# Optimization experiments

Hardware: AMD Instinct MI355X
Metric: run time of the kernel (lower is better)

Reference implementation:

```python
import jax, jax.numpy as jnp
import numpy as np

NUM_PRODUCT = 100000
NUM_USERS = 10000
EMBED_DIM = 512
H = EMBED_DIM // 2          # gru_hidden_size = embedding_dim // 2
MBS = 20                    # max_basket_size
NB = 64                     # baskets per user
K = 256                     # batch of users
B = NB * MBS                # flattened item positions per user
L = 2                       # GRU layers


def setup_inputs() -> dict:
    key = jax.random.key(0)
    ks = jax.random.split(key, 8)
    filter_basket_prob = jax.random.uniform(ks[0], (K, B), dtype=jnp.float32)
    # item ids in [-1, NUM_PRODUCT-1]; -1 is padding (shifted to padding_idx 0)
    input_seq_tensor = jax.random.randint(ks[1], (K, B), 0, NUM_PRODUCT + 1) - 1
    uid = jax.random.randint(ks[2], (K,), 0, NUM_USERS)
    embed_table = 0.02 * jax.random.normal(ks[3], (NUM_PRODUCT + 1, H), dtype=jnp.float32)
    embed_table = embed_table.at[0].set(0.0)  # padding_idx=0
    s = 1.0 / np.sqrt(H)
    w_ih = jax.random.uniform(ks[4], (L, 3 * H, H), jnp.float32, -s, s)
    w_hh = jax.random.uniform(ks[5], (L, 3 * H, H), jnp.float32, -s, s)
    b_ih = jax.random.uniform(ks[6], (L, 3 * H), jnp.float32, -s, s)
    b_hh = jax.random.uniform(ks[7], (L, 3 * H), jnp.float32, -s, s)
    return {"filter_basket_prob": filter_basket_prob, "input_seq_tensor": input_seq_tensor,
            "uid": uid, "embed_table": embed_table,
            "w_ih": w_ih, "w_hh": w_hh, "b_ih": b_ih, "b_hh": b_hh}


def _gru_layer(x, wih, whh, bih, bhh):
    # x: [K, T, H]; torch GRU gate math (r, z, n gate order)
    gi = jnp.einsum('kth,gh->ktg', x, wih) + bih  # [K, T, 3H]

    def step(h, gi_t):
        gh = h @ whh.T + bhh
        ir, iz, inn = jnp.split(gi_t, 3, axis=-1)
        hr, hz, hn = jnp.split(gh, 3, axis=-1)
        r = jax.nn.sigmoid(ir + hr)
        z = jax.nn.sigmoid(iz + hz)
        n = jnp.tanh(inn + r * hn)
        h_new = (1.0 - z) * n + z * h
        return h_new, h_new

    h0 = jnp.zeros((x.shape[0], whh.shape[1]), x.dtype)
    _, hs = jax.lax.scan(step, h0, jnp.swapaxes(gi, 0, 1))  # [T, K, H]
    return jnp.swapaxes(hs, 0, 1)


def reference(filter_basket_prob, input_seq_tensor, uid, embed_table, w_ih, w_hh, b_ih, b_hh):
    Kb, Bb = filter_basket_prob.shape
    Hh = embed_table.shape[1]
    nb = Bb // MBS
    # mask out padding positions (constant w.r.t. grads, as in torch .detach())
    mask = (input_seq_tensor != -1).astype(jnp.float32)
    prob = filter_basket_prob * mask                      # [K, B]
    emb = embed_table[input_seq_tensor + 1]               # [K, B, H]
    emb_f = (emb * prob[..., None]).reshape(Kb, nb, MBS, Hh)
    prob_b = prob.reshape(Kb, nb, MBS)
    filter_b = prob_b.max(axis=-1)                        # [K, NB]
    # avg basket pooling: sum(prob*emb) / (sum(prob) + eps)
    basket_emb = emb_f.sum(axis=2) / (prob_b.sum(axis=-1, keepdims=True) + 1e-10)
    valid = (filter_b > 0).astype(jnp.int32)
    # stable descending sort moves valid baskets to the front, preserving order
    order = jnp.argsort(-valid, axis=-1)                  # [K, NB]
    lengths = valid.sum(axis=-1)
    lengths = lengths + (lengths == 0).astype(lengths.dtype)  # clamp to >= 1
    x = jnp.take_along_axis(basket_emb, order[:, :, None], axis=1)  # [K, NB, H]
    # pack/pad/unsort in the original cancel out: GRU output at t depends only
    # on inputs <= t, so run the full padded scan and read step lengths-1.
    for l in range(w_ih.shape[0]):
        x = _gru_layer(x, w_ih[l], w_hh[l], b_ih[l], b_hh[l])
    return x[jnp.arange(Kb), lengths - 1]                 # [K, H]
```

## Files before the change

### kernel.cpp

```cpp
#include <hip/hip_runtime.h>
#include <cstdint>

#define KU 256
#define NBASK 64
#define MBS 20
#define BITEMS 1280
#define HD 256
#define G3 768
#define TT 64

typedef short v8s __attribute__((ext_vector_type(8)));
typedef float v4f __attribute__((ext_vector_type(4)));
typedef unsigned short v4us __attribute__((ext_vector_type(4)));
typedef unsigned int v4u __attribute__((ext_vector_type(4)));

__device__ __forceinline__ unsigned short f2b(float f){
  uint32_t u = __float_as_uint(f);
  u += 0x7FFFu + ((u >> 16) & 1u);
  return (unsigned short)(u >> 16);
}
__device__ __forceinline__ float b2f(unsigned short s){
  return __uint_as_float(((uint32_t)s) << 16);
}
__device__ __forceinline__ unsigned int packf(float x){
  unsigned short hi = f2b(x);
  unsigned short lo = f2b(x - b2f(hi));
  return ((unsigned int)hi << 16) | lo;
}
__device__ __forceinline__ float unpackf(unsigned int v){
  return b2f((unsigned short)(v >> 16)) + b2f((unsigned short)(v & 0xffffu));
}

__global__ __launch_bounds__(1024) void k_convert(
    const float* __restrict__ wih, const float* __restrict__ whh,
    unsigned short* __restrict__ wih1hi, unsigned short* __restrict__ wih1lo,
    unsigned short* __restrict__ wih2hi, unsigned short* __restrict__ wih2lo,
    unsigned short* __restrict__ whh1hi, unsigned short* __restrict__ whh1lo,
    unsigned short* __restrict__ whh2hi, unsigned short* __restrict__ whh2lo)
{
  int idx = blockIdx.x * 1024 + threadIdx.x;
  int which = blockIdx.y;
  float v;
  if (which == 0)      v = wih[idx];
  else if (which == 1) v = wih[196608 + idx];
  else if (which == 2) v = whh[idx];
  else                 v = whh[196608 + idx];
  unsigned short hi = f2b(v);
  unsigned short lo = f2b(v - b2f(hi));
  if (which == 0)      { wih1hi[idx] = hi; wih1lo[idx] = lo; }
  else if (which == 1) { wih2hi[idx] = hi; wih2lo[idx] = lo; }
  else if (which == 2) { whh1hi[idx] = hi; whh1lo[idx] = lo; }
  else                 { whh2hi[idx] = hi; whh2lo[idx] = lo; }
}

__global__ void k_zero(int* flags){
  if (threadIdx.x < 32) flags[threadIdx.x] = 0;
}

__global__ __launch_bounds__(64) void k_order(
    const float* __restrict__ prob, const int* __restrict__ seq,
    int* __restrict__ order, int* __restrict__ lengths)
{
  int k = blockIdx.x, j = threadIdx.x;
  int base = k * BITEMS + j * MBS;
  float mx = 0.f;
  #pragma unroll
  for (int m = 0; m < MBS; m++) {
    int it = seq[base + m];
    float p = (it >= 0) ? prob[base + m] : 0.f;
    mx = fmaxf(mx, p);
  }
  bool valid = mx > 0.f;
  unsigned long long bal = __ballot(valid);
  int len = __popcll(bal);
  unsigned long long below = bal & ((1ull << j) - 1ull);
  int pos = valid ? __popcll(below) : (len + (j - __popcll(below)));
  order[k * NBASK + j] = pos;
  if (j == 0) lengths[k] = (len > 0) ? len : 1;
}

__global__ __launch_bounds__(256) void k_basket(
    const float* __restrict__ prob, const int* __restrict__ seq,
    const float* __restrict__ table, const int* __restrict__ order,
    unsigned short* __restrict__ xbhi, unsigned short* __restrict__ xblo)
{
  int j = blockIdx.x, k = blockIdx.y;
  int h = threadIdx.x;
  int base = k * BITEMS + j * MBS;
  float acc = 0.f, sp = 0.f;
  #pragma unroll
  for (int m = 0; m < MBS; m++) {
    int it = seq[base + m];
    if (it >= 0) {
      float p = prob[base + m];
      sp += p;
      acc += p * table[(size_t)(it + 1) * HD + h];
    }
  }
  float val = acc / (sp + 1e-10f);
  int dest = order[k * NBASK + j];
  unsigned short hi = f2b(val);
  size_t o = ((size_t)k * NBASK + dest) * HD + h;
  xbhi[o] = hi;
  xblo[o] = f2b(val - b2f(hi));
}

__global__ __launch_bounds__(256) void k_gemm3(
    const unsigned short* __restrict__ Xhi, const unsigned short* __restrict__ Xlo,
    const unsigned short* __restrict__ Whi, const unsigned short* __restrict__ Wlo,
    const float* __restrict__ bias, float* __restrict__ Y)
{
  int nblk = blockIdx.x;
  int mblk = blockIdx.y;
  int wv = threadIdx.x >> 6;
  int l = threadIdx.x & 63;
  int r = l & 15, g = l >> 4;
  int mbase = mblk * 64 + wv * 16;
  int nbase = nblk * 64;
  v4f acc[4];
  #pragma unroll
  for (int c = 0; c < 4; c++) {
    float bn = bias[nbase + c * 16 + r];
    acc[c] = (v4f){bn, bn, bn, bn};
  }
  const unsigned short* xh = Xhi + (size_t)(mbase + r) * HD;
  const unsigned short* xl = Xlo + (size_t)(mbase + r) * HD;
  #pragma unroll
  for (int k0 = 0; k0 < HD; k0 += 32) {
    v8s ahi = *(const v8s*)(xh + k0 + g * 8);
    v8s alo = *(const v8s*)(xl + k0 + g * 8);
    #pragma unroll
    for (int c = 0; c < 4; c++) {
      size_t wo = (size_t)(nbase + c * 16 + r) * HD + k0 + g * 8;
      v8s bhi = *(const v8s*)(Whi + wo);
      v8s blo = *(const v8s*)(Wlo + wo);
      acc[c] = __builtin_amdgcn_mfma_f32_16x16x32_bf16(ahi, bhi, acc[c], 0, 0, 0);
      acc[c] = __builtin_amdgcn_mfma_f32_16x16x32_bf16(alo, bhi, acc[c], 0, 0, 0);
      acc[c] = __builtin_amdgcn_mfma_f32_16x16x32_bf16(ahi, blo, acc[c], 0, 0, 0);
    }
  }
  #pragma unroll
  for (int c = 0; c < 4; c++) {
    int n = nbase + c * 16 + r;
    int mrow = mbase + g * 4;
    #pragma unroll
    for (int i = 0; i < 4; i++)
      Y[(size_t)(mrow + i) * G3 + n] = acc[c][i];
  }
}

__device__ __forceinline__ void mfma_phase(
    const unsigned short* __restrict__ w0, const unsigned short* __restrict__ w1,
    const unsigned short* __restrict__ w2,
    const unsigned short (*h_hi)[256], const unsigned short (*h_lo)[256],
    const unsigned short* nlo_s, int r, int g, int j,
    v4f& a0, v4f& a1, v4f& a2)
{
  v8s cw0[3], cw1[3], cw2[3];
  #pragma unroll
  for (int p = 0; p < 3; p++) {
    cw0[p] = *(const v8s*)(w0 + p * 32);
    cw1[p] = *(const v8s*)(w1 + p * 32);
    cw2[p] = *(const v8s*)(w2 + p * 32);
  }
  #pragma unroll
  for (int kk = 0; kk < 8; kk++) {
    int buf = kk % 3;
    int slotA = ((kk * 4 + g) ^ (r & 7)) * 8;
    v8s ahi = *(const v8s*)&h_hi[r][slotA];
    v8s alo = *(const v8s*)&h_lo[r][slotA];
    v8s nl  = *(const v8s*)&nlo_s[j * 256 + slotA];
    v8s u0 = cw0[buf], u1 = cw1[buf], u2 = cw2[buf];
    if (kk + 3 < 8) {
      cw0[buf] = *(const v8s*)(w0 + (kk + 3) * 32);
      cw1[buf] = *(const v8s*)(w1 + (kk + 3) * 32);
      cw2[buf] = *(const v8s*)(w2 + (kk + 3) * 32);
    }
    a0 = __builtin_amdgcn_mfma_f32_16x16x32_bf16(ahi, u0, a0, 0, 0, 0);
    a0 = __builtin_amdgcn_mfma_f32_16x16x32_bf16(alo, u0, a0, 0, 0, 0);
    a1 = __builtin_amdgcn_mfma_f32_16x16x32_bf16(ahi, u1, a1, 0, 0, 0);
    a1 = __builtin_amdgcn_mfma_f32_16x16x32_bf16(alo, u1, a1, 0, 0, 0);
    a2 = __builtin_amdgcn_mfma_f32_16x16x32_bf16(ahi, u2, a2, 0, 0, 0);
    a2 = __builtin_amdgcn_mfma_f32_16x16x32_bf16(alo, u2, a2, 0, 0, 0);
    a2 = __builtin_amdgcn_mfma_f32_16x16x32_bf16(ahi, nl, a2, 0, 0, 0);
  }
}

__global__ __launch_bounds__(1024) void k_pipeline(
    const unsigned short* __restrict__ whh1hi, const unsigned short* __restrict__ whh1lo,
    const unsigned short* __restrict__ wih2hi, const unsigned short* __restrict__ wih2lo,
    const unsigned short* __restrict__ whh2hi, const unsigned short* __restrict__ whh2lo,
    float* __restrict__ gi, unsigned int* __restrict__ h1pk,
    const float* __restrict__ bhh1, const float* __restrict__ bih2,
    const float* __restrict__ bhh2,
    const int* __restrict__ lengths, float* __restrict__ out, int* flags)
{
  __shared__ unsigned short h_hi[16][256], h_lo[16][256];
  __shared__ unsigned short nlo_s[65536];
  int tid = threadIdx.x;
  int l = tid & 63, r = l & 15, g = l >> 4;
  int swv = __builtin_amdgcn_readfirstlane(tid >> 6);
  int role = blockIdx.x >> 4, b = blockIdx.x & 15;
  int ub = b * 16;
  int j = swv * 16 + r;
  int* aflag = flags;
  int* gflag = flags + 16;

  const unsigned short* whi_g = (role == 0) ? whh1hi : (role == 1) ? wih2hi : whh2hi;
  const unsigned short* wlo_g = (role == 0) ? whh1lo : (role == 1) ? wih2lo : whh2lo;

  for (int idx = tid; idx < 4096; idx += 1024) {
    ((unsigned short*)h_hi)[idx] = 0;
    ((unsigned short*)h_lo)[idx] = 0;
  }
  const unsigned short* wlo_n = wlo_g + 2 * 65536;
  for (int idx = tid; idx < 65536; idx += 1024) {
    int row = idx >> 8, col = idx & 255;
    int slot = (col >> 3) ^ (row & 7);
    nlo_s[row * 256 + slot * 8 + (col & 7)] = wlo_n[idx];
  }
  const unsigned short* w0 = whi_g + (size_t)j * 256 + g * 8;
  const unsigned short* w1 = w0 + 65536;
  const unsigned short* w2 = w0 + 131072;
  __syncthreads();

  if (role == 0) {
    float b_r = bhh1[j], b_z = bhh1[256 + j], b_n = bhh1[512 + j];
    const float* gp[4];
    #pragma unroll
    for (int i = 0; i < 4; i++)
      gp[i] = gi + (size_t)(ub + g * 4 + i) * TT * G3 + j;
    float hold[4] = {0.f, 0.f, 0.f, 0.f};
    for (int t = 0; t < TT; t++) {
      float gir[4], giz[4], gin[4];
      #pragma unroll
      for (int i = 0; i < 4; i++) {
        gir[i] = gp[i][0]; giz[i] = gp[i][256]; gin[i] = gp[i][512];
        gp[i] += G3;
      }
      v4f a0 = {0.f,0.f,0.f,0.f}, a1 = {0.f,0.f,0.f,0.f}, a2 = {0.f,0.f,0.f,0.f};
      mfma_phase(w0, w1, w2, h_hi, h_lo, nlo_s, r, g, j, a0, a1, a2);
      __syncthreads();
      #pragma unroll
      for (int i = 0; i < 4; i++) {
        float hr = a0[i] + b_r, hz = a1[i] + b_z, hn = a2[i] + b_n;
        float rr = 1.f / (1.f + __expf(-(gir[i] + hr)));
        float zz = 1.f / (1.f + __expf(-(giz[i] + hz)));
        float e  = __expf(2.f * (gin[i] + rr * hn));
        float nn = 1.f - 2.f / (e + 1.f);
        float hnew = (1.f - zz) * nn + zz * hold[i];
        hold[i] = hnew;
        unsigned short h_  = f2b(hnew);
        unsigned short lo_ = f2b(hnew - b2f(h_));
        int u = g * 4 + i;
        int pos = (((j >> 3) ^ (u & 7)) << 3) + (j & 7);
        h_hi[u][pos] = h_;
        h_lo[u][pos] = lo_;
        h1pk[((size_t)(ub + u) * TT + t) * HD + j] = ((unsigned int)h_ << 16) | lo_;
      }
      __syncthreads();
      if (tid == 0) {
        __threadfence();
        __hip_atomic_store(&aflag[b], t + 1, __ATOMIC_RELEASE, __HIP_MEMORY_SCOPE_AGENT);
      }
    }
  } else if (role == 1) {
    float b_r = bih2[j], b_z = bih2[256 + j], b_n = bih2[512 + j];
    int uu = tid >> 6, q4 = tid & 63, j0 = q4 * 4;
    int slotW = (((j0 >> 3) ^ (uu & 7)) << 3) + (j0 & 7);
    unsigned int* gi_u = (unsigned int*)gi;
    for (int t = 0; t < TT; t++) {
      if (tid == 0)
        while (__hip_atomic_load(&aflag[b], __ATOMIC_ACQUIRE, __HIP_MEMORY_SCOPE_AGENT) < t + 1)
          __builtin_amdgcn_s_sleep(8);
      __syncthreads();
      v4u pk = *(const v4u*)(h1pk + ((size_t)(ub + uu) * TT + t) * HD + j0);
      v4us hv, lv;
      #pragma unroll
      for (int i = 0; i < 4; i++) {
        hv[i] = (unsigned short)(pk[i] >> 16);
        lv[i] = (unsigned short)(pk[i] & 0xffffu);
      }
      *(v4us*)&h_hi[uu][slotW] = hv;
      *(v4us*)&h_lo[uu][slotW] = lv;
      __syncthreads();
      v4f a0 = {b_r, b_r, b_r, b_r}, a1 = {b_z, b_z, b_z, b_z}, a2 = {b_n, b_n, b_n, b_n};
      mfma_phase(w0, w1, w2, h_hi, h_lo, nlo_s, r, g, j, a0, a1, a2);
      #pragma unroll
      for (int i = 0; i < 4; i++) {
        int u2 = g * 4 + i;
        size_t base = ((size_t)(ub + u2) * TT + t) * G3;
        gi_u[base + j]       = packf(a0[i]);
        gi_u[base + 256 + j] = packf(a1[i]);
        gi_u[base + 512 + j] = packf(a2[i]);
      }
      __syncthreads();
      if (tid == 0) {
        __threadfence();
        __hip_atomic_store(&gflag[b], t + 1, __ATOMIC_RELEASE, __HIP_MEMORY_SCOPE_AGENT);
      }
    }
  } else {
    float b_r = bhh2[j], b_z = bhh2[256 + j], b_n = bhh2[512 + j];
    const unsigned int* gp[4];
    int lenr[4];
    #pragma unroll
    for (int i = 0; i < 4; i++) {
      gp[i] = (const unsigned int*)gi + (size_t)(ub + g * 4 + i) * TT * G3 + j;
      lenr[i] = lengths[ub + g * 4 + i];
    }
    float hold[4] = {0.f, 0.f, 0.f, 0.f};
    for (int t = 0; t < TT; t++) {
      if (tid == 0)
        while (__hip_atomic_load(&gflag[b], __ATOMIC_ACQUIRE, __HIP_MEMORY_SCOPE_AGENT) < t + 1)
          __builtin_amdgcn_s_sleep(8);
      __syncthreads();
      unsigned int vr[4], vz[4], vn[4];
      #pragma unroll
      for (int i = 0; i < 4; i++) {
        vr[i] = gp[i][0]; vz[i] = gp[i][256]; vn[i] = gp[i][512];
        gp[i] += G3;
      }
      v4f a0 = {0.f,0.f,0.f,0.f}, a1 = {0.f,0.f,0.f,0.f}, a2 = {0.f,0.f,0.f,0.f};
      mfma_phase(w0, w1, w2, h_hi, h_lo, nlo_s, r, g, j, a0, a1, a2);
      __syncthreads();
      #pragma unroll
      for (int i = 0; i < 4; i++) {
        float hr = a0[i] + b_r, hz = a1[i] + b_z, hn = a2[i] + b_n;
        float rr = 1.f / (1.f + __expf(-(unpackf(vr[i]) + hr)));
        float zz = 1.f / (1.f + __expf(-(unpackf(vz[i]) + hz)));
        float e  = __expf(2.f * (unpackf(vn[i]) + rr * hn));
        float nn = 1.f - 2.f / (e + 1.f);
        float hnew = (1.f - zz) * nn + zz * hold[i];
        hold[i] = hnew;
        unsigned short h_  = f2b(hnew);
        unsigned short lo_ = f2b(hnew - b2f(h_));
        int u = g * 4 + i;
        int pos = (((j >> 3) ^ (u & 7)) << 3) + (j & 7);
        h_hi[u][pos] = h_;
        h_lo[u][pos] = lo_;
        if (t == lenr[i] - 1)
          out[(size_t)(ub + u) * HD + j] = hnew;
      }
      __syncthreads();
    }
  }
}

extern "C" void kernel_launch(void* const* d_in, const int* in_sizes, int n_in,
                              void* d_out, int out_size, void* d_ws, size_t ws_size,
                              hipStream_t stream) {
  const float* prob  = (const float*)d_in[0];
  const int*   seq   = (const int*)d_in[1];
  const float* table = (const float*)d_in[3];
  const float* wih   = (const float*)d_in[4];
  const float* whh   = (const float*)d_in[5];
  const float* bih   = (const float*)d_in[6];
  const float* bhh   = (const float*)d_in[7];
  float* out = (float*)d_out;

  char* ws = (char*)d_ws;
  float* gi            = (float*)ws;
  unsigned short* xbhi = (unsigned short*)(ws + 50331648);
  unsigned short* xblo = (unsigned short*)(ws + 58720256);
  unsigned int* h1pk   = (unsigned int*)xbhi;
  char* wsw = ws + 67108864;
  const size_t WSZ = 393216;
  unsigned short* wih1hi = (unsigned short*)(wsw + 0 * WSZ);
  unsigned short* wih1lo = (unsigned short*)(wsw + 1 * WSZ);
  unsigned short* wih2hi = (unsigned short*)(wsw + 2 * WSZ);
  unsigned short* wih2lo = (unsigned short*)(wsw + 3 * WSZ);
  unsigned short* whh1hi = (unsigned short*)(wsw + 4 * WSZ);
  unsigned short* whh1lo = (unsigned short*)(wsw + 5 * WSZ);
  unsigned short* whh2hi = (unsigned short*)(wsw + 6 * WSZ);
  unsigned short* whh2lo = (unsigned short*)(wsw + 7 * WSZ);
  int* order   = (int*)(wsw + 8 * WSZ);
  int* lengths = order + KU * NBASK;
  int* flags   = lengths + KU;

  k_zero<<<1, 64, 0, stream>>>(flags);
  k_convert<<<dim3(192, 4), 1024, 0, stream>>>(wih, whh,
      wih1hi, wih1lo, wih2hi, wih2lo, whh1hi, whh1lo, whh2hi, whh2lo);
  k_order<<<dim3(KU), 64, 0, stream>>>(prob, seq, order, lengths);
  k_basket<<<dim3(NBASK, KU), 256, 0, stream>>>(prob, seq, table, order, xbhi, xblo);
  k_gemm3<<<dim3(12, 256), 256, 0, stream>>>(xbhi, xblo, wih1hi, wih1lo, bih, gi);
  k_pipeline<<<dim3(48), 1024, 0, stream>>>(
      whh1hi, whh1lo, wih2hi, wih2lo, whh2hi, whh2lo,
      gi, h1pk, bhh, bih + G3, bhh + G3, lengths, out, flags);
}
```

Measured before the change: 832.6 us.

## Split each GRU pipeline role across two half-hidden blocks with sibling flag exchange

The persistent 48-block, 1024-thread pipeline becomes 96 blocks of 512 threads, so each user group's recurrent work is split across two blocks that each own half of the hidden units. Each block does the K-half of its MFMA that uses its own h from the previous step first, then waits on the sibling's flag and pulls the other half of h through global memory (h1pk / a new h2x buffer) before the second half. This doubles the number of CUs on the serial recurrence and hides the cross-block exchange behind compute. The cost is an extra global handshake every step, shorter polling sleeps, and h2x reusing the wih1hi workspace after the gemm.

```diff
diff --git a/kernel.cpp b/kernel.cpp
--- a/kernel.cpp
+++ b/kernel.cpp
@@ -29,6 +29,10 @@
 }
 __device__ __forceinline__ float unpackf(unsigned int v){
   return b2f((unsigned short)(v >> 16)) + b2f((unsigned short)(v & 0xffffu));
+}
+__device__ __forceinline__ void waitflag(int* f, int v){
+  while (__hip_atomic_load(f, __ATOMIC_ACQUIRE, __HIP_MEMORY_SCOPE_AGENT) < v)
+    __builtin_amdgcn_s_sleep(2);
 }
 
 __global__ __launch_bounds__(1024) void k_convert(
@@ -54,7 +58,7 @@
 }
 
 __global__ void k_zero(int* flags){
-  if (threadIdx.x < 32) flags[threadIdx.x] = 0;
+  if (threadIdx.x < 96) flags[threadIdx.x] = 0;
 }
 
 __global__ __launch_bounds__(64) void k_order(
@@ -149,32 +153,42 @@
   }
 }
 
-__device__ __forceinline__ void mfma_phase(
+__device__ __forceinline__ void wprologue(
+    const unsigned short* w0, const unsigned short* w1, const unsigned short* w2,
+    int half4, v8s (&cw0)[3], v8s (&cw1)[3], v8s (&cw2)[3])
+{
+  #pragma unroll
+  for (int q = 0; q < 3; q++) {
+    int p = (half4 + q) & 7;
+    cw0[q] = *(const v8s*)(w0 + p * 32);
+    cw1[q] = *(const v8s*)(w1 + p * 32);
+    cw2[q] = *(const v8s*)(w2 + p * 32);
+  }
+}
+template<int K0>
+__device__ __forceinline__ void mfma_quad(
     const unsigned short* __restrict__ w0, const unsigned short* __restrict__ w1,
     const unsigned short* __restrict__ w2,
     const unsigned short (*h_hi)[256], const unsigned short (*h_lo)[256],
-    const unsigned short* nlo_s, int r, int g, int j,
+    const unsigned short* __restrict__ nlo_s, int r, int g, int jloc, int half4,
+    v8s (&cw0)[3], v8s (&cw1)[3], v8s (&cw2)[3],
     v4f& a0, v4f& a1, v4f& a2)
 {
-  v8s cw0[3], cw1[3], cw2[3];
-  #pragma unroll
-  for (int p = 0; p < 3; p++) {
-    cw0[p] = *(const v8s*)(w0 + p * 32);
-    cw1[p] = *(const v8s*)(w1 + p * 32);
-    cw2[p] = *(const v8s*)(w2 + p * 32);
-  }
-  #pragma unroll
-  for (int kk = 0; kk < 8; kk++) {
-    int buf = kk % 3;
-    int slotA = ((kk * 4 + g) ^ (r & 7)) * 8;
+  #pragma unroll
+  for (int q = 0; q < 4; q++) {
+    int kidx = K0 + q;
+    int buf = kidx % 3;
+    int p = (half4 + kidx) & 7;
+    int slotA = ((p * 4 + g) ^ (r & 7)) * 8;
     v8s ahi = *(const v8s*)&h_hi[r][slotA];
     v8s alo = *(const v8s*)&h_lo[r][slotA];
-    v8s nl  = *(const v8s*)&nlo_s[j * 256 + slotA];
+    v8s nl  = *(const v8s*)&nlo_s[jloc * 256 + slotA];
     v8s u0 = cw0[buf], u1 = cw1[buf], u2 = cw2[buf];
-    if (kk + 3 < 8) {
-      cw0[buf] = *(const v8s*)(w0 + (kk + 3) * 32);
-      cw1[buf] = *(const v8s*)(w1 + (kk + 3) * 32);
-      cw2[buf] = *(const v8s*)(w2 + (kk + 3) * 32);
+    if (kidx + 3 < 8) {
+      int p3 = (half4 + kidx + 3) & 7;
+      cw0[buf] = *(const v8s*)(w0 + p3 * 32);
+      cw1[buf] = *(const v8s*)(w1 + p3 * 32);
+      cw2[buf] = *(const v8s*)(w2 + p3 * 32);
     }
     a0 = __builtin_amdgcn_mfma_f32_16x16x32_bf16(ahi, u0, a0, 0, 0, 0);
     a0 = __builtin_amdgcn_mfma_f32_16x16x32_bf16(alo, u0, a0, 0, 0, 0);
@@ -186,35 +200,38 @@
   }
 }
 
-__global__ __launch_bounds__(1024) void k_pipeline(
+__global__ __launch_bounds__(512) void k_pipe(
     const unsigned short* __restrict__ whh1hi, const unsigned short* __restrict__ whh1lo,
     const unsigned short* __restrict__ wih2hi, const unsigned short* __restrict__ wih2lo,
     const unsigned short* __restrict__ whh2hi, const unsigned short* __restrict__ whh2lo,
-    float* __restrict__ gi, unsigned int* __restrict__ h1pk,
+    float* __restrict__ gi, unsigned int* __restrict__ h1pk, unsigned int* __restrict__ h2x,
     const float* __restrict__ bhh1, const float* __restrict__ bih2,
     const float* __restrict__ bhh2,
     const int* __restrict__ lengths, float* __restrict__ out, int* flags)
 {
   __shared__ unsigned short h_hi[16][256], h_lo[16][256];
-  __shared__ unsigned short nlo_s[65536];
+  __shared__ unsigned short nlo_s[40960];
   int tid = threadIdx.x;
   int l = tid & 63, r = l & 15, g = l >> 4;
   int swv = __builtin_amdgcn_readfirstlane(tid >> 6);
-  int role = blockIdx.x >> 4, b = blockIdx.x & 15;
+  int bx = blockIdx.x;
+  int role = bx >> 5, sub = bx & 31, half = sub >> 4, b = sub & 15;
+  int half4 = half * 4;
   int ub = b * 16;
-  int j = swv * 16 + r;
-  int* aflag = flags;
-  int* gflag = flags + 16;
+  int jloc = swv * 16 + r, j = half * 128 + jloc;
+  int* aflag = flags, *gflag = flags + 32, *bflag = flags + 64;
+  int myf = sub, sibf = sub ^ 16;
 
   const unsigned short* whi_g = (role == 0) ? whh1hi : (role == 1) ? wih2hi : whh2hi;
   const unsigned short* wlo_g = (role == 0) ? whh1lo : (role == 1) ? wih2lo : whh2lo;
-
-  for (int idx = tid; idx < 4096; idx += 1024) {
+  const float* bb_ = (role == 0) ? bhh1 : (role == 1) ? bih2 : bhh2;
+
+  for (int idx = tid; idx < 4096; idx += 512) {
     ((unsigned short*)h_hi)[idx] = 0;
     ((unsigned short*)h_lo)[idx] = 0;
   }
-  const unsigned short* wlo_n = wlo_g + 2 * 65536;
-  for (int idx = tid; idx < 65536; idx += 1024) {
+  const unsigned short* wlo_n = wlo_g + 2 * 65536 + half * 128 * 256;
+  for (int idx = tid; idx < 32768; idx += 512) {
     int row = idx >> 8, col = idx & 255;
     int slot = (col >> 3) ^ (row & 7);
     nlo_s[row * 256 + slot * 8 + (col & 7)] = wlo_n[idx];
@@ -222,15 +239,20 @@
   const unsigned short* w0 = whi_g + (size_t)j * 256 + g * 8;
   const unsigned short* w1 = w0 + 65536;
   const unsigned short* w2 = w0 + 131072;
+  float b_r = bb_[j], b_z = bb_[256 + j], b_n = bb_[512 + j];
+  int sibbase = (1 - half) * 128;
+  int xu = tid >> 5;
   __syncthreads();
 
   if (role == 0) {
-    float b_r = bhh1[j], b_z = bhh1[256 + j], b_n = bhh1[512 + j];
+    float hold[4] = {0.f, 0.f, 0.f, 0.f};
     const float* gp[4];
+    unsigned int* hq[4];
     #pragma unroll
-    for (int i = 0; i < 4; i++)
+    for (int i = 0; i < 4; i++) {
       gp[i] = gi + (size_t)(ub + g * 4 + i) * TT * G3 + j;
-    float hold[4] = {0.f, 0.f, 0.f, 0.f};
+      hq[i] = h1pk + (size_t)(ub + g * 4 + i) * TT * HD + j;
+    }
     for (int t = 0; t < TT; t++) {
       float gir[4], giz[4], gin[4];
       #pragma unroll
@@ -238,9 +260,24 @@
         gir[i] = gp[i][0]; giz[i] = gp[i][256]; gin[i] = gp[i][512];
         gp[i] += G3;
       }
+      v8s cw0[3], cw1[3], cw2[3];
+      wprologue(w0, w1, w2, half4, cw0, cw1, cw2);
       v4f a0 = {0.f,0.f,0.f,0.f}, a1 = {0.f,0.f,0.f,0.f}, a2 = {0.f,0.f,0.f,0.f};
-      mfma_phase(w0, w1, w2, h_hi, h_lo, nlo_s, r, g, j, a0, a1, a2);
-      __syncthreads();
+      mfma_quad<0>(w0, w1, w2, h_hi, h_lo, nlo_s, r, g, jloc, half4, cw0, cw1, cw2, a0, a1, a2);
+      if (t > 0 && tid == 0) waitflag(&aflag[sibf], t);
+      __syncthreads();
+      if (t > 0) {
+        int sj = sibbase + (tid & 31) * 4;
+        v4u pk = *(const v4u*)&h1pk[((size_t)(ub + xu) * TT + (t - 1)) * HD + sj];
+        int pos = (((sj >> 3) ^ (xu & 7)) << 3) + (sj & 7);
+        v4us hv, lv;
+        #pragma unroll
+        for (int i = 0; i < 4; i++) { hv[i] = (unsigned short)(pk[i] >> 16); lv[i] = (unsigned short)(pk[i] & 0xffffu); }
+        *(v4us*)&h_hi[xu][pos] = hv;
+        *(v4us*)&h_lo[xu][pos] = lv;
+      }
+      __syncthreads();
+      mfma_quad<4>(w0, w1, w2, h_hi, h_lo, nlo_s, r, g, jloc, half4, cw0, cw1, cw2, a0, a1, a2);
       #pragma unroll
       for (int i = 0; i < 4; i++) {
         float hr = a0[i] + b_r, hz = a1[i] + b_z, hn = a2[i] + b_n;
@@ -256,40 +293,44 @@
         int pos = (((j >> 3) ^ (u & 7)) << 3) + (j & 7);
         h_hi[u][pos] = h_;
         h_lo[u][pos] = lo_;
-        h1pk[((size_t)(ub + u) * TT + t) * HD + j] = ((unsigned int)h_ << 16) | lo_;
+        hq[i][0] = ((unsigned int)h_ << 16) | lo_;
+        hq[i] += HD;
       }
       __syncthreads();
       if (tid == 0) {
         __threadfence();
-        __hip_atomic_store(&aflag[b], t + 1, __ATOMIC_RELEASE, __HIP_MEMORY_SCOPE_AGENT);
+        __hip_atomic_store(&aflag[myf], t + 1, __ATOMIC_RELEASE, __HIP_MEMORY_SCOPE_AGENT);
       }
     }
   } else if (role == 1) {
-    float b_r = bih2[j], b_z = bih2[256 + j], b_n = bih2[512 + j];
-    int uu = tid >> 6, q4 = tid & 63, j0 = q4 * 4;
-    int slotW = (((j0 >> 3) ^ (uu & 7)) << 3) + (j0 & 7);
     unsigned int* gi_u = (unsigned int*)gi;
     for (int t = 0; t < TT; t++) {
-      if (tid == 0)
-        while (__hip_atomic_load(&aflag[b], __ATOMIC_ACQUIRE, __HIP_MEMORY_SCOPE_AGENT) < t + 1)
-          __builtin_amdgcn_s_sleep(8);
-      __syncthreads();
-      v4u pk = *(const v4u*)(h1pk + ((size_t)(ub + uu) * TT + t) * HD + j0);
-      v4us hv, lv;
+      if (tid == 0) { waitflag(&aflag[b], t + 1); waitflag(&aflag[16 + b], t + 1); }
+      __syncthreads();
+      {
+        int c0 = (tid & 31) * 8;
+        const unsigned int* src = &h1pk[((size_t)(ub + xu) * TT + t) * HD + c0];
+        #pragma unroll
+        for (int hf = 0; hf < 2; hf++) {
+          v4u pk = *(const v4u*)(src + hf * 4);
+          int sj = c0 + hf * 4;
+          int pos = (((sj >> 3) ^ (xu & 7)) << 3) + (sj & 7);
+          v4us hv, lv;
+          #pragma unroll
+          for (int i = 0; i < 4; i++) { hv[i] = (unsigned short)(pk[i] >> 16); lv[i] = (unsigned short)(pk[i] & 0xffffu); }
+          *(v4us*)&h_hi[xu][pos] = hv;
+          *(v4us*)&h_lo[xu][pos] = lv;
+        }
+      }
+      __syncthreads();
+      v8s cw0[3], cw1[3], cw2[3];
+      wprologue(w0, w1, w2, half4, cw0, cw1, cw2);
+      v4f a0 = {b_r, b_r, b_r, b_r}, a1 = {b_z, b_z, b_z, b_z}, a2 = {b_n, b_n, b_n, b_n};
+      mfma_quad<0>(w0, w1, w2, h_hi, h_lo, nlo_s, r, g, jloc, half4, cw0, cw1, cw2, a0, a1, a2);
+      mfma_quad<4>(w0, w1, w2, h_hi, h_lo, nlo_s, r, g, jloc, half4, cw0, cw1, cw2, a0, a1, a2);
       #pragma unroll
       for (int i = 0; i < 4; i++) {
-        hv[i] = (unsigned short)(pk[i] >> 16);
-        lv[i] = (unsigned short)(pk[i] & 0xffffu);
-      }
-      *(v4us*)&h_hi[uu][slotW] = hv;
-      *(v4us*)&h_lo[uu][slotW] = lv;
-      __syncthreads();
-      v4f a0 = {b_r, b_r, b_r, b_r}, a1 = {b_z, b_z, b_z, b_z}, a2 = {b_n, b_n, b_n, b_n};
-      mfma_phase(w0, w1, w2, h_hi, h_lo, nlo_s, r, g, j, a0, a1, a2);
-      #pragma unroll
-      for (int i = 0; i < 4; i++) {
-        int u2 = g * 4 + i;
-        size_t base = ((size_t)(ub + u2) * TT + t) * G3;
+        size_t base = ((size_t)(ub + g * 4 + i) * TT + t) * G3;
         gi_u[base + j]       = packf(a0[i]);
         gi_u[base + 256 + j] = packf(a1[i]);
         gi_u[base + 512 + j] = packf(a2[i]);
@@ -297,33 +338,46 @@
       __syncthreads();
       if (tid == 0) {
         __threadfence();
-        __hip_atomic_store(&gflag[b], t + 1, __ATOMIC_RELEASE, __HIP_MEMORY_SCOPE_AGENT);
+        __hip_atomic_store(&gflag[myf], t + 1, __ATOMIC_RELEASE, __HIP_MEMORY_SCOPE_AGENT);
       }
     }
   } else {
-    float b_r = bhh2[j], b_z = bhh2[256 + j], b_n = bhh2[512 + j];
-    const unsigned int* gp[4];
+    float hold[4] = {0.f, 0.f, 0.f, 0.f};
+    const unsigned int* gq[4];
     int lenr[4];
     #pragma unroll
     for (int i = 0; i < 4; i++) {
-      gp[i] = (const unsigned int*)gi + (size_t)(ub + g * 4 + i) * TT * G3 + j;
+      gq[i] = (const unsigned int*)gi + (size_t)(ub + g * 4 + i) * TT * G3 + j;
       lenr[i] = lengths[ub + g * 4 + i];
     }
-    float hold[4] = {0.f, 0.f, 0.f, 0.f};
     for (int t = 0; t < TT; t++) {
-      if (tid == 0)
-        while (__hip_atomic_load(&gflag[b], __ATOMIC_ACQUIRE, __HIP_MEMORY_SCOPE_AGENT) < t + 1)
-          __builtin_amdgcn_s_sleep(8);
-      __syncthreads();
+      v8s cw0[3], cw1[3], cw2[3];
+      wprologue(w0, w1, w2, half4, cw0, cw1, cw2);
+      v4f a0 = {0.f,0.f,0.f,0.f}, a1 = {0.f,0.f,0.f,0.f}, a2 = {0.f,0.f,0.f,0.f};
+      mfma_quad<0>(w0, w1, w2, h_hi, h_lo, nlo_s, r, g, jloc, half4, cw0, cw1, cw2, a0, a1, a2);
+      if (tid == 0) {
+        waitflag(&gflag[myf], t + 1);
+        if (t > 0) waitflag(&bflag[sibf], t);
+      }
+      __syncthreads();
+      if (t > 0) {
+        int sj = sibbase + (tid & 31) * 4;
+        v4u pk = *(const v4u*)&h2x[(size_t)(ub + xu) * HD + sj];
+        int pos = (((sj >> 3) ^ (xu & 7)) << 3) + (sj & 7);
+        v4us hv, lv;
+        #pragma unroll
+        for (int i = 0; i < 4; i++) { hv[i] = (unsigned short)(pk[i] >> 16); lv[i] = (unsigned short)(pk[i] & 0xffffu); }
+        *(v4us*)&h_hi[xu][pos] = hv;
+        *(v4us*)&h_lo[xu][pos] = lv;
+      }
       unsigned int vr[4], vz[4], vn[4];
       #pragma unroll
       for (int i = 0; i < 4; i++) {
-        vr[i] = gp[i][0]; vz[i] = gp[i][256]; vn[i] = gp[i][512];
-        gp[i] += G3;
-      }
-      v4f a0 = {0.f,0.f,0.f,0.f}, a1 = {0.f,0.f,0.f,0.f}, a2 = {0.f,0.f,0.f,0.f};
-      mfma_phase(w0, w1, w2, h_hi, h_lo, nlo_s, r, g, j, a0, a1, a2);
-      __syncthreads();
+        vr[i] = gq[i][0]; vz[i] = gq[i][256]; vn[i] = gq[i][512];
+        gq[i] += G3;
+      }
+      __syncthreads();
+      mfma_quad<4>(w0, w1, w2, h_hi, h_lo, nlo_s, r, g, jloc, half4, cw0, cw1, cw2, a0, a1, a2);
       #pragma unroll
       for (int i = 0; i < 4; i++) {
         float hr = a0[i] + b_r, hz = a1[i] + b_z, hn = a2[i] + b_n;
@@ -339,10 +393,15 @@
         int pos = (((j >> 3) ^ (u & 7)) << 3) + (j & 7);
         h_hi[u][pos] = h_;
         h_lo[u][pos] = lo_;
+        h2x[(size_t)(ub + u) * HD + j] = ((unsigned int)h_ << 16) | lo_;
         if (t == lenr[i] - 1)
           out[(size_t)(ub + u) * HD + j] = hnew;
       }
       __syncthreads();
+      if (tid == 0) {
+        __threadfence();
+        __hip_atomic_store(&bflag[myf], t + 1, __ATOMIC_RELEASE, __HIP_MEMORY_SCOPE_AGENT);
+      }
     }
   }
 }
@@ -377,14 +436,15 @@
   int* order   = (int*)(wsw + 8 * WSZ);
   int* lengths = order + KU * NBASK;
   int* flags   = lengths + KU;
-
-  k_zero<<<1, 64, 0, stream>>>(flags);
+  unsigned int* h2x = (unsigned int*)wih1hi;
+
+  k_zero<<<1, 128, 0, stream>>>(flags);
   k_convert<<<dim3(192, 4), 1024, 0, stream>>>(wih, whh,
       wih1hi, wih1lo, wih2hi, wih2lo, whh1hi, whh1lo, whh2hi, whh2lo);
   k_order<<<dim3(KU), 64, 0, stream>>>(prob, seq, order, lengths);
   k_basket<<<dim3(NBASK, KU), 256, 0, stream>>>(prob, seq, table, order, xbhi, xblo);
   k_gemm3<<<dim3(12, 256), 256, 0, stream>>>(xbhi, xblo, wih1hi, wih1lo, bih, gi);
-  k_pipeline<<<dim3(48), 1024, 0, stream>>>(
+  k_pipe<<<dim3(96), 512, 0, stream>>>(
       whh1hi, whh1lo, wih2hi, wih2lo, whh2hi, whh2lo,
-      gi, h1pk, bhh, bih + G3, bhh + G3, lengths, out, flags);
-}
+      gi, h1pk, h2x, bhh, bih + G3, bhh + G3, lengths, out, flags);
+}
```

Result: faster. 712.3 us (-14.4%).
